# Kernel tuning notes

Hardware: AMD Instinct MI355X
Metric: run time of the kernel (lower is better)

## Reference

```python
import jax, jax.numpy as jnp
import numpy as np

# dims from VideoTokenizerConfig defaults + chosen video shape
B, T, IH, IW, C = 2, 16, 224, 224, 3
TP, PS, D, DFF, L, NH, K = 4, 16, 512, 2048, 6, 8, 8192
Tp, Hp, Wp = T // TP, IH // PS, IW // PS   # 4, 14, 14
S = Tp * Hp * Wp                           # 784 tokens
PIN = TP * PS * PS * C                     # 3072 patch elements
COMMIT = 0.25


def _ln(x, s, b):
    m = x.mean(-1, keepdims=True)
    v = ((x - m) ** 2).mean(-1, keepdims=True)
    return (x - m) / jnp.sqrt(v + 1e-6) * s + b


def _mha(x, Wqkv, bqkv, Wo, bo):
    b_, s_, d_ = x.shape
    hd = d_ // NH
    q = (x @ Wqkv[0] + bqkv[0]).reshape(b_, s_, NH, hd)
    k = (x @ Wqkv[1] + bqkv[1]).reshape(b_, s_, NH, hd)
    v = (x @ Wqkv[2] + bqkv[2]).reshape(b_, s_, NH, hd)
    att = jax.nn.softmax(jnp.einsum('bqhd,bkhd->bhqk', q, k) / jnp.sqrt(jnp.float32(hd)), axis=-1)
    o = jnp.einsum('bhqk,bkhd->bqhd', att, v).reshape(b_, s_, d_)
    return o @ Wo + bo


def _blocks(z, ln1s, ln1b, Wqkv, bqkv, Wo, bo, ln2s, ln2b, W1, b1, W2, b2):
    for i in range(L):  # small fixed layer count
        z = z + _mha(_ln(z, ln1s[i], ln1b[i]), Wqkv[i], bqkv[i], Wo[i], bo[i])
        h = jax.nn.gelu(_ln(z, ln2s[i], ln2b[i]) @ W1[i] + b1[i])
        z = z + h @ W2[i] + b2[i]
    return z


def _forward(video, e_patch_W, e_patch_b, e_pos_t, e_pos_h, e_pos_w,
             e_ln1_s, e_ln1_b, e_Wqkv, e_bqkv, e_Wo, e_bo, e_ln2_s, e_ln2_b,
             e_W1, e_b1, e_W2, e_b2, e_lnf_s, e_lnf_b, e_cb_W, e_cb_b,
             codebook,
             d_cb_W, d_cb_b, d_pos_t, d_pos_h, d_pos_w,
             d_ln1_s, d_ln1_b, d_Wqkv, d_bqkv, d_Wo, d_bo, d_ln2_s, d_ln2_b,
             d_W1, d_b1, d_W2, d_b2, d_lnf_s, d_lnf_b, d_px_W, d_px_b):
    # ---- encoder: 3D patchify ----
    v = video.reshape(B, Tp, TP, Hp, PS, Wp, PS, C)
    v = v.transpose(0, 1, 3, 5, 2, 4, 6, 7).reshape(B, Tp, Hp, Wp, PIN)
    z = v @ e_patch_W + e_patch_b
    z = z + e_pos_t + e_pos_h + e_pos_w
    z = z.reshape(B, S, D)
    z = _blocks(z, e_ln1_s, e_ln1_b, e_Wqkv, e_bqkv, e_Wo, e_bo,
                e_ln2_s, e_ln2_b, e_W1, e_b1, e_W2, e_b2)
    z = _ln(z, e_lnf_s, e_lnf_b)
    z_e = z @ e_cb_W + e_cb_b                      # [B,S,D]
    # ---- VQ quantize ----
    flat = z_e.reshape(-1, D)                      # [B*S, D]
    d2 = (flat ** 2).sum(1, keepdims=True) + (codebook ** 2).sum(1) - 2.0 * flat @ codebook.T
    idx = jnp.argmin(d2, axis=1)                   # [B*S]
    z_q = codebook[idx].reshape(z_e.shape)
    commit = jnp.mean((jax.lax.stop_gradient(z_q) - z_e) ** 2)
    cb_loss = jnp.mean((z_q - jax.lax.stop_gradient(z_e)) ** 2)
    z_q = z_e + jax.lax.stop_gradient(z_q - z_e)   # straight-through
    counts = jnp.zeros((K,), flat.dtype).at[idx].add(1.0)
    p = counts / idx.shape[0]                      # == mean(one_hot, axis=0)
    perplexity = jnp.exp(-jnp.sum(p * jnp.log(p + 1e-10)))
    # ---- decoder ----
    zd = z_q.reshape(B, Tp, Hp, Wp, D) @ d_cb_W + d_cb_b
    zd = zd + d_pos_t + d_pos_h + d_pos_w
    zd = zd.reshape(B, S, D)
    zd = _blocks(zd, d_ln1_s, d_ln1_b, d_Wqkv, d_bqkv, d_Wo, d_bo,
                 d_ln2_s, d_ln2_b, d_W1, d_b1, d_W2, d_b2)
    zd = _ln(zd, d_lnf_s, d_lnf_b)
    px = zd.reshape(B, Tp, Hp, Wp, D) @ d_px_W + d_px_b
    px = px.reshape(B, Tp, Hp, Wp, TP, PS, PS, C)
    recon = px.transpose(0, 1, 4, 2, 5, 3, 6, 7).reshape(B, T, IH, IW, C)
    return recon, idx.reshape(B, Tp, Hp, Wp), commit, cb_loss, perplexity


def setup_inputs() -> dict:
    key = jax.random.key(0)
    ks = iter(jax.random.split(key, 48))
    def nrm(shape, s=0.02):
        return (s * jax.random.normal(next(ks), shape)).astype(jnp.float32)
    z = lambda shape: jnp.zeros(shape, jnp.float32)
    o = lambda shape: jnp.ones(shape, jnp.float32)
    inp = {}
    inp['video'] = jax.random.normal(next(ks), (B, T, IH, IW, C), jnp.float32)
    # encoder params
    inp['e_patch_W'] = nrm((PIN, D)); inp['e_patch_b'] = z((D,))
    inp['e_pos_t'] = nrm((1, Tp, 1, 1, D)); inp['e_pos_h'] = nrm((1, 1, Hp, 1, D)); inp['e_pos_w'] = nrm((1, 1, 1, Wp, D))
    inp['e_ln1_s'] = o((L, D)); inp['e_ln1_b'] = z((L, D))
    inp['e_Wqkv'] = nrm((L, 3, D, D)); inp['e_bqkv'] = z((L, 3, D))
    inp['e_Wo'] = nrm((L, D, D)); inp['e_bo'] = z((L, D))
    inp['e_ln2_s'] = o((L, D)); inp['e_ln2_b'] = z((L, D))
    inp['e_W1'] = nrm((L, D, DFF)); inp['e_b1'] = z((L, DFF))
    inp['e_W2'] = nrm((L, DFF, D)); inp['e_b2'] = z((L, D))
    inp['e_lnf_s'] = o((D,)); inp['e_lnf_b'] = z((D,))
    inp['e_cb_W'] = nrm((D, D)); inp['e_cb_b'] = z((D,))
    inp['codebook'] = nrm((K, D))
    # decoder params
    inp['d_cb_W'] = nrm((D, D)); inp['d_cb_b'] = z((D,))
    inp['d_pos_t'] = nrm((1, Tp, 1, 1, D)); inp['d_pos_h'] = nrm((1, 1, Hp, 1, D)); inp['d_pos_w'] = nrm((1, 1, 1, Wp, D))
    inp['d_ln1_s'] = o((L, D)); inp['d_ln1_b'] = z((L, D))
    inp['d_Wqkv'] = nrm((L, 3, D, D)); inp['d_bqkv'] = z((L, 3, D))
    inp['d_Wo'] = nrm((L, D, D)); inp['d_bo'] = z((L, D))
    inp['d_ln2_s'] = o((L, D)); inp['d_ln2_b'] = z((L, D))
    inp['d_W1'] = nrm((L, D, DFF)); inp['d_b1'] = z((L, DFF))
    inp['d_W2'] = nrm((L, DFF, D)); inp['d_b2'] = z((L, D))
    inp['d_lnf_s'] = o((D,)); inp['d_lnf_b'] = z((D,))
    inp['d_px_W'] = nrm((D, PIN)); inp['d_px_b'] = z((PIN,))
    return inp


def reference(video, e_patch_W, e_patch_b, e_pos_t, e_pos_h, e_pos_w,
              e_ln1_s, e_ln1_b, e_Wqkv, e_bqkv, e_Wo, e_bo, e_ln2_s, e_ln2_b,
              e_W1, e_b1, e_W2, e_b2, e_lnf_s, e_lnf_b, e_cb_W, e_cb_b,
              codebook,
              d_cb_W, d_cb_b, d_pos_t, d_pos_h, d_pos_w,
              d_ln1_s, d_ln1_b, d_Wqkv, d_bqkv, d_Wo, d_bo, d_ln2_s, d_ln2_b,
              d_W1, d_b1, d_W2, d_b2, d_lnf_s, d_lnf_b, d_px_W, d_px_b):
    return _forward(video, e_patch_W, e_patch_b, e_pos_t, e_pos_h, e_pos_w,
                    e_ln1_s, e_ln1_b, e_Wqkv, e_bqkv, e_Wo, e_bo, e_ln2_s, e_ln2_b,
                    e_W1, e_b1, e_W2, e_b2, e_lnf_s, e_lnf_b, e_cb_W, e_cb_b,
                    codebook,
                    d_cb_W, d_cb_b, d_pos_t, d_pos_h, d_pos_w,
                    d_ln1_s, d_ln1_b, d_Wqkv, d_bqkv, d_Wo, d_bo, d_ln2_s, d_ln2_b,
                    d_W1, d_b1, d_W2, d_b2, d_lnf_s, d_lnf_b, d_px_W, d_px_b)
```

## Files before the change

### kernel.cpp

```cpp
#include <hip/hip_runtime.h>
#include <math.h>

#define Bq    2
#define Dq    512
#define DFFq  2048
#define Lq    6
#define NHq   8
#define HDq   64
#define Kq    8192
#define Sq    784
#define PINq  3072
#define TOKq  1568
#define RECN  4816896L

#define OFF_BIG  0L
#define SZ_BIG   12845056L
#define OFF_Z    (OFF_BIG + SZ_BIG)
#define OFF_XLN  (OFF_Z    + 802816L)
#define OFF_QKV  (OFF_XLN  + 802816L)
#define OFF_ATTO (OFF_QKV  + 2408448L)
#define OFF_H    (OFF_ATTO + 802816L)
#define OFF_ZE   (OFF_H    + 3211264L)
#define OFF_ZQ   (OFF_ZE   + 802816L)
#define OFF_CN   (OFF_ZQ   + 802816L)
#define OFF_IDX  (OFF_CN   + 8192L)
#define OFF_CNT  (OFF_IDX  + 1568L)
#define OFF_PART (OFF_CNT  + 8192L)
#define OFF_MIN  (OFF_PART + 1568L)
#define OFF_END  (OFF_MIN  + 3136L)

#define CEXT 802816L

typedef short bf16x8 __attribute__((ext_vector_type(8)));
typedef float f32x4  __attribute__((ext_vector_type(4)));
typedef unsigned short u16;
typedef unsigned long long u64;

#define XLO 802816L
#define QLO 2408448L
#define ALO 802816L
#define HLO 3211264L
#define PLO 4816896L
#define ZLO 802816L
#define CBLO 4194304L

__device__ __forceinline__ float wave_sum(float v) {
    #pragma unroll
    for (int o = 32; o; o >>= 1) v += __shfl_xor(v, o);
    return v;
}
__device__ __forceinline__ float gelu_f(float x) {
    float u = 0.7978845608028654f * (x + 0.044715f * x * x * x);
    float a = fabsf(u);
    float t = __expf(-2.0f * a);
    float th = (1.0f - t) / (1.0f + t);
    th = copysignf(th, u);
    return 0.5f * x * (1.0f + th);
}
__device__ __forceinline__ void split_f32(float x, u16& h, u16& l) {
    unsigned u = __float_as_uint(x);
    unsigned t = u + 0x7fffu + ((u >> 16) & 1u);
    h = (u16)(t >> 16);
    float r = x - __uint_as_float((t >> 16) << 16);
    l = (u16)(__float_as_uint(r) >> 16);
}
__device__ __forceinline__ void gload16(const u16* g, u16* l) {
    __builtin_amdgcn_global_load_lds(
        (const __attribute__((address_space(1))) void*)g,
        (__attribute__((address_space(3))) void*)l,
        16, 0, 0);
}

__global__ __launch_bounds__(256)
void wconv_t(const float* __restrict__ W, int ldw, int Kd,
             u16* __restrict__ WT, long loT, long soW, long soT)
{
    __shared__ u16 Lh[32][33], Ll[32][33];
    const float* Wp = W + (long)blockIdx.z * soW;
    u16* Tp = WT + (long)blockIdx.z * soT;
    int k0 = blockIdx.x << 5, n0 = blockIdx.y << 5;
    int t = threadIdx.x;
    int r = t >> 3, c4 = (t & 7) << 2;
    float4 v = *(const float4*)(Wp + (long)(k0 + r) * ldw + n0 + c4);
    u16 h, l;
    split_f32(v.x, h, l); Lh[c4+0][r] = h; Ll[c4+0][r] = l;
    split_f32(v.y, h, l); Lh[c4+1][r] = h; Ll[c4+1][r] = l;
    split_f32(v.z, h, l); Lh[c4+2][r] = h; Ll[c4+2][r] = l;
    split_f32(v.w, h, l); Lh[c4+3][r] = h; Ll[c4+3][r] = l;
    __syncthreads();
    int n = t >> 3, kc = (t & 7) << 2;
    u16* dst = Tp + (long)(n0 + n) * Kd + k0 + kc;
    u16 oh[4] = {Lh[n][kc], Lh[n][kc+1], Lh[n][kc+2], Lh[n][kc+3]};
    u16 ol[4] = {Ll[n][kc], Ll[n][kc+1], Ll[n][kc+2], Ll[n][kc+3]};
    *(uint2*)dst = *(uint2*)oh;
    *(uint2*)(dst + loT) = *(uint2*)ol;
}

__global__ __launch_bounds__(256)
void wconv4(const float* __restrict__ Wqkv, const float* __restrict__ Wo,
            const float* __restrict__ W1, const float* __restrict__ W2,
            u16* __restrict__ dst)
{
    __shared__ u16 Lh[32][33], Ll[32][33];
    int id = blockIdx.x;
    const float* W; int ldw, Kd, kblk, nblk; u16* Tp; long loT;
    if (id < 768) {
        int z = id >> 8, rid = id & 255;
        kblk = rid & 15; nblk = rid >> 4;
        W = Wqkv + (long)z * 262144; ldw = 512; Kd = 512;
        Tp = dst + (long)z * 262144; loT = 786432;
    } else if (id < 1024) {
        int rid = id - 768; kblk = rid & 15; nblk = rid >> 4;
        W = Wo; ldw = 512; Kd = 512; Tp = dst + 1572864; loT = 262144;
    } else if (id < 2048) {
        int rid = id - 1024; kblk = rid & 15; nblk = rid >> 4;
        W = W1; ldw = 2048; Kd = 512; Tp = dst + 2097152; loT = 1048576;
    } else {
        int rid = id - 2048; kblk = rid & 63; nblk = rid >> 6;
        W = W2; ldw = 512; Kd = 2048; Tp = dst + 4194304; loT = 1048576;
    }
    int k0 = kblk << 5, n0 = nblk << 5;
    int t = threadIdx.x;
    int r = t >> 3, c4 = (t & 7) << 2;
    float4 v = *(const float4*)(W + (long)(k0 + r) * ldw + n0 + c4);
    u16 h, l;
    split_f32(v.x, h, l); Lh[c4+0][r] = h; Ll[c4+0][r] = l;
    split_f32(v.y, h, l); Lh[c4+1][r] = h; Ll[c4+1][r] = l;
    split_f32(v.z, h, l); Lh[c4+2][r] = h; Ll[c4+2][r] = l;
    split_f32(v.w, h, l); Lh[c4+3][r] = h; Ll[c4+3][r] = l;
    __syncthreads();
    int n = t >> 3, kc = (t & 7) << 2;
    u16* d = Tp + (long)(n0 + n) * Kd + k0 + kc;
    u16 oh[4] = {Lh[n][kc], Lh[n][kc+1], Lh[n][kc+2], Lh[n][kc+3]};
    u16 ol[4] = {Ll[n][kc], Ll[n][kc+1], Ll[n][kc+2], Ll[n][kc+3]};
    *(uint2*)d = *(uint2*)oh;
    *(uint2*)(d + loT) = *(uint2*)ol;
}

__global__ __launch_bounds__(256)
void splitp(const float* __restrict__ X, u16* __restrict__ Y, long lo, long n4)
{
    long i = (long)blockIdx.x * 256 + threadIdx.x;
    if (i >= n4) return;
    float4 v = *(const float4*)(X + i * 4);
    u16 h[4], l[4];
    split_f32(v.x, h[0], l[0]); split_f32(v.y, h[1], l[1]);
    split_f32(v.z, h[2], l[2]); split_f32(v.w, h[3], l[3]);
    *(uint2*)(Y + i * 4) = *(uint2*)h;
    *(uint2*)(Y + lo + i * 4) = *(uint2*)l;
}

template<int MATH, int LV>
__global__ __launch_bounds__(256)
void gemm_bb(const u16* __restrict__ A, long rsA, long loA, long soA, long siA,
             const u16* __restrict__ B, long rsB, long loB, long soB, long siB,
             const float* __restrict__ bias, long siBias,
             const float* __restrict__ extra,
             float* __restrict__ Cf, int ldc, long soC, long siC,
             u16* __restrict__ Cb, int rsC, long loC,
             float* __restrict__ part, long pstride,
             int M, int N, int K, float alpha,
             int bdiv, int ksplit, int klen, int gx)
{
    constexpr int OFF_BH = (LV >= 2) ? 8192 : 4096;
    __shared__ u16 SH[LV == 3 ? 16384 : (LV == 2 ? 12288 : 8192)];
    const int zb2 = blockIdx.z;
    const int zk = zb2 % ksplit, zb = zb2 / ksplit;
    const int zo = zb / bdiv, zi = zb - zo * bdiv;
    A += zo * soA + zi * siA;
    B += zo * soB + zi * siB;
    const float* bi = bias ? bias + zi * siBias : nullptr;

    const int nwg = gridDim.x;
    int orig = blockIdx.x;
    int qq = nwg >> 3, rr = nwg & 7;
    int xcd = orig & 7, sidx = orig >> 3;
    int wgid = (xcd < rr ? xcd * (qq + 1) : rr * (qq + 1) + (xcd - rr) * qq) + sidx;
    const int m0 = (wgid % gx) << 6, n0 = (wgid / gx) << 6;

    const int t = threadIdx.x;
    const int kbeg = zk * klen;
    int kend = kbeg + klen; if (kend > K) kend = K;

    const int w = t >> 6, lane = t & 63;
    const int wm = w >> 1, wn = w & 1;
    const int l15 = lane & 15, g = lane >> 4;
    const int wq = w << 9;

    const int csrc = ((t & 3) + ((t >> 3) & 7)) & 3;
    int arow = m0 + (t >> 2); if (arow > M - 1) arow = M - 1;
    const u16* Apr = A + (long)arow * rsA + (csrc << 3);
    const u16* Bpr = B + (long)(n0 + (t >> 2)) * rsB + (csrc << 3);

    f32x4 acc[2][2] = {};

    for (int k0 = kbeg; k0 < kend; k0 += 64) {
        gload16(Apr + k0,            &SH[wq]);
        if (LV >= 2) gload16(Apr + k0 + loA,      &SH[4096 + wq]);
        gload16(Bpr + k0,            &SH[OFF_BH + wq]);
        if (LV == 3) gload16(Bpr + k0 + loB, &SH[12288 + wq]);
        gload16(Apr + k0 + 32,       &SH[2048 + wq]);
        if (LV >= 2) gload16(Apr + k0 + 32 + loA, &SH[4096 + 2048 + wq]);
        gload16(Bpr + k0 + 32,       &SH[OFF_BH + 2048 + wq]);
        if (LV == 3) gload16(Bpr + k0 + 32 + loB, &SH[12288 + 2048 + wq]);
        __syncthreads();

        #pragma unroll
        for (int sub = 0; sub < 2; ++sub) {
            const int so = sub << 11;
            bf16x8 ah[2], al2[2], bh2[2], bl2[2];
            #pragma unroll
            for (int mi = 0; mi < 2; ++mi) {
                int row = (wm << 5) + (mi << 4) + l15;
                int off = (row << 5) + (((g - (row >> 1)) & 3) << 3);
                ah[mi]  = *(const bf16x8*)&SH[so + off];
                if (LV >= 2) al2[mi] = *(const bf16x8*)&SH[4096 + so + off];
            }
            #pragma unroll
            for (int ni = 0; ni < 2; ++ni) {
                int row = (wn << 5) + (ni << 4) + l15;
                int off = (row << 5) + (((g - (row >> 1)) & 3) << 3);
                bh2[ni] = *(const bf16x8*)&SH[OFF_BH + so + off];
                if (LV == 3) bl2[ni] = *(const bf16x8*)&SH[12288 + so + off];
            }
            #pragma unroll
            for (int mi = 0; mi < 2; ++mi)
                #pragma unroll
                for (int ni = 0; ni < 2; ++ni) {
                    acc[mi][ni] = __builtin_amdgcn_mfma_f32_16x16x32_bf16(ah[mi], bh2[ni], acc[mi][ni], 0, 0, 0);
                    if (LV == 3) acc[mi][ni] = __builtin_amdgcn_mfma_f32_16x16x32_bf16(ah[mi], bl2[ni], acc[mi][ni], 0, 0, 0);
                    if (LV >= 2) acc[mi][ni] = __builtin_amdgcn_mfma_f32_16x16x32_bf16(al2[mi], bh2[ni], acc[mi][ni], 0, 0, 0);
                }
        }
        __syncthreads();
    }

    if (ksplit > 1) {
        float* P = part + (long)zk * pstride + zo * soC + zi * siC;
        #pragma unroll
        for (int mi = 0; mi < 2; ++mi)
            #pragma unroll
            for (int ni = 0; ni < 2; ++ni) {
                int gn = n0 + (wn << 5) + (ni << 4) + l15;
                if (gn >= N) continue;
                int gmb = m0 + (wm << 5) + (mi << 4) + (g << 2);
                #pragma unroll
                for (int r = 0; r < 4; ++r) {
                    int gm = gmb + r;
                    if (gm < M) P[(long)gm * ldc + gn] = acc[mi][ni][r];
                }
            }
        return;
    }
    if (MATH == 0) {
        float* Co = Cf + zo * soC + zi * siC;
        #pragma unroll
        for (int mi = 0; mi < 2; ++mi)
            #pragma unroll
            for (int ni = 0; ni < 2; ++ni) {
                int gn = n0 + (wn << 5) + (ni << 4) + l15;
                if (gn >= N) continue;
                int gmb = m0 + (wm << 5) + (mi << 4) + (g << 2);
                #pragma unroll
                for (int r = 0; r < 4; ++r) {
                    int gm = gmb + r;
                    if (gm >= M) continue;
                    Co[(long)gm * ldc + gn] = alpha * acc[mi][ni][r] + (bi ? bi[gn] : 0.0f);
                }
            }
    } else {
        u16* Cu = Cb + zo * soC + zi * siC;
        #pragma unroll
        for (int mi = 0; mi < 2; ++mi)
            #pragma unroll
            for (int ni = 0; ni < 2; ++ni) {
                int gn = n0 + (wn << 5) + (ni << 4) + l15;
                if (gn >= N) continue;
                int gmb = m0 + (wm << 5) + (mi << 4) + (g << 2);
                #pragma unroll
                for (int r = 0; r < 4; ++r) {
                    int gm = gmb + r;
                    if (gm >= M) continue;
                    float v = acc[mi][ni][r] + bi[gn];
                    if (MATH == 2) v = gelu_f(v);
                    u16 h, l; split_f32(v, h, l);
                    Cu[(long)gm * rsC + gn] = h;
                    Cu[(long)gm * rsC + gn + loC] = l;
                }
            }
    }
}

__global__ __launch_bounds__(256)
void gemm_d2w(const u16* __restrict__ A, long rsA, long loA,
              const u16* __restrict__ B, long rsB, long loB,
              const float* __restrict__ extra, u64* __restrict__ mb,
              int M, int N, int K, int gx)
{
    __shared__ u16 SH[24576];
    const int nwg = gridDim.x;
    int orig = blockIdx.x;
    int qq = nwg >> 3, rr = nwg & 7;
    int xcd = orig & 7, sidx = orig >> 3;
    int wgid = (xcd < rr ? xcd * (qq + 1) : rr * (qq + 1) + (xcd - rr) * qq) + sidx;
    const int m0 = (wgid % gx) << 6, n0 = (wgid / gx) << 7;

    const int t = threadIdx.x;
    const int w = t >> 6, lane = t & 63;
    const int wm = w >> 1, wn = w & 1;
    const int l15 = lane & 15, g = lane >> 4;
    const int wq = w << 9;

    const int csrc = ((t & 3) + ((t >> 3) & 7)) & 3;
    int arow = m0 + (t >> 2); if (arow > M - 1) arow = M - 1;
    const u16* Apr = A + (long)arow * rsA + (csrc << 3);
    const u16* Bpr0 = B + (long)(n0 + (t >> 2)) * rsB + (csrc << 3);
    const u16* Bpr1 = B + (long)(n0 + 64 + (t >> 2)) * rsB + (csrc << 3);

    f32x4 acc[2][4] = {};

    for (int k0 = 0; k0 < K; k0 += 64) {
        gload16(Apr + k0,             &SH[wq]);
        gload16(Apr + k0 + 32,        &SH[2048 + wq]);
        gload16(Apr + k0 + loA,       &SH[4096 + wq]);
        gload16(Apr + k0 + 32 + loA,  &SH[4096 + 2048 + wq]);
        gload16(Bpr0 + k0,            &SH[8192 + wq]);
        gload16(Bpr1 + k0,            &SH[8192 + 2048 + wq]);
        gload16(Bpr0 + k0 + 32,       &SH[12288 + wq]);
        gload16(Bpr1 + k0 + 32,       &SH[12288 + 2048 + wq]);
        gload16(Bpr0 + k0 + loB,      &SH[16384 + wq]);
        gload16(Bpr1 + k0 + loB,      &SH[16384 + 2048 + wq]);
        gload16(Bpr0 + k0 + 32 + loB, &SH[20480 + wq]);
        gload16(Bpr1 + k0 + 32 + loB, &SH[20480 + 2048 + wq]);
        __syncthreads();

        #pragma unroll
        for (int sub = 0; sub < 2; ++sub) {
            const int soA = sub << 11;
            const int soB = sub << 12;
            bf16x8 ah[2], al2[2], bh2[4], bl2[4];
            #pragma unroll
            for (int mi = 0; mi < 2; ++mi) {
                int row = (wm << 5) + (mi << 4) + l15;
                int off = (row << 5) + (((g - (row >> 1)) & 3) << 3);
                ah[mi]  = *(const bf16x8*)&SH[soA + off];
                al2[mi] = *(const bf16x8*)&SH[4096 + soA + off];
            }
            #pragma unroll
            for (int ni = 0; ni < 4; ++ni) {
                int row = (wn << 6) + (ni << 4) + l15;
                int off = (row << 5) + (((g - (row >> 1)) & 3) << 3);
                bh2[ni] = *(const bf16x8*)&SH[8192 + soB + off];
                bl2[ni] = *(const bf16x8*)&SH[16384 + soB + off];
            }
            #pragma unroll
            for (int mi = 0; mi < 2; ++mi)
                #pragma unroll
                for (int ni = 0; ni < 4; ++ni) {
                    acc[mi][ni] = __builtin_amdgcn_mfma_f32_16x16x32_bf16(ah[mi],  bh2[ni], acc[mi][ni], 0, 0, 0);
                    acc[mi][ni] = __builtin_amdgcn_mfma_f32_16x16x32_bf16(ah[mi],  bl2[ni], acc[mi][ni], 0, 0, 0);
                    acc[mi][ni] = __builtin_amdgcn_mfma_f32_16x16x32_bf16(al2[mi], bh2[ni], acc[mi][ni], 0, 0, 0);
                }
        }
        __syncthreads();
    }

    #pragma unroll
    for (int mi = 0; mi < 2; ++mi) {
        #pragma unroll
        for (int r = 0; r < 4; ++r) {
            u64 best = 0xFFFFFFFFFFFFFFFFULL;
            #pragma unroll
            for (int ni = 0; ni < 4; ++ni) {
                int gn = n0 + (wn << 6) + (ni << 4) + l15;
                float v = extra[gn] - 2.0f * acc[mi][ni][r];
                unsigned ub = __float_as_uint(v);
                ub = ub ^ ((ub >> 31) ? 0xFFFFFFFFu : 0x80000000u);
                u64 pk = ((u64)ub << 32) | (unsigned)gn;
                best = pk < best ? pk : best;
            }
            #pragma unroll
            for (int sft = 1; sft <= 8; sft <<= 1) {
                u64 o = __shfl_xor(best, sft);
                best = o < best ? o : best;
            }
            if (l15 == 0) {
                int gm = m0 + (wm << 5) + (mi << 4) + (g << 2) + r;
                if (gm < M) atomicMin(&mb[gm], best);
            }
        }
    }
}

#define KP 72
#define VP 40
#define CHR 196
template<bool X2>
__global__ __launch_bounds__(256)
void flash_kernel(const u16* __restrict__ qkv, float* __restrict__ O4, float* __restrict__ ML)
{
    __shared__ u16 Kh[32 * KP], Kl[32 * KP];
    __shared__ u16 Vh[64 * VP], Vl[64 * VP];
    __shared__ u16 Ph[64 * VP], Pl[64 * VP];

    const int qb = blockIdx.x, bh = blockIdx.y, ch = blockIdx.z;
    const int b = bh >> 3, h = bh & 7;
    const int jbeg = ch * CHR, jend = jbeg + CHR;
    const int t = threadIdx.x, w = t >> 6, lane = t & 63;
    const int l15 = lane & 15, g = lane >> 4;
    const long base = (long)b * 784 * 1536;
    const u16* Qg = qkv + base + h * 64;
    const u16* Kg = qkv + base + 512 + h * 64;
    const u16* Vg = qkv + base + 1024 + h * 64;

    const int q0 = qb << 6;
    int qr = q0 + w * 16 + l15; if (qr > 783) qr = 783;
    const u16* Qp = Qg + (long)qr * 1536 + g * 8;
    bf16x8 qh[2], ql[2];
    qh[0] = *(const bf16x8*)(Qp);
    qh[1] = *(const bf16x8*)(Qp + 32);
    ql[0] = *(const bf16x8*)(Qp + QLO);
    ql[1] = *(const bf16x8*)(Qp + QLO + 32);

    f32x4 O[4] = {};
    float m_[4] = {-1e30f, -1e30f, -1e30f, -1e30f};
    float l_[4] = {};

    const int srow = t >> 3, sc = (t & 7) << 3;

    for (int j0 = jbeg; j0 < jend; j0 += 32) {
        {
            int jr = j0 + srow;
            if (jr < jend) {
                const u16* Kp = Kg + (long)jr * 1536 + sc;
                *(uint4*)&Kh[srow * KP + sc] = *(const uint4*)(Kp);
                if (!X2) *(uint4*)&Kl[srow * KP + sc] = *(const uint4*)(Kp + QLO);
                const u16* Vp = Vg + (long)jr * 1536 + sc;
                u16 th[8], tl[8];
                *(uint4*)th = *(const uint4*)Vp;
                if (!X2) *(uint4*)tl = *(const uint4*)(Vp + QLO);
                #pragma unroll
                for (int e = 0; e < 8; ++e) {
                    Vh[(sc + e) * VP + srow] = th[e];
                    if (!X2) Vl[(sc + e) * VP + srow] = tl[e];
                }
            } else {
                uint4 zz = {0, 0, 0, 0};
                *(uint4*)&Kh[srow * KP + sc] = zz;
                if (!X2) *(uint4*)&Kl[srow * KP + sc] = zz;
                #pragma unroll
                for (int e = 0; e < 8; ++e) {
                    Vh[(sc + e) * VP + srow] = 0;
                    if (!X2) Vl[(sc + e) * VP + srow] = 0;
                }
            }
        }
        __syncthreads();

        f32x4 S[2] = {};
        #pragma unroll
        for (int f = 0; f < 2; ++f) {
            #pragma unroll
            for (int ks = 0; ks < 2; ++ks) {
                bf16x8 kh = *(const bf16x8*)&Kh[(f * 16 + l15) * KP + ks * 32 + g * 8];
                S[f] = __builtin_amdgcn_mfma_f32_16x16x32_bf16(qh[ks], kh, S[f], 0, 0, 0);
                if (!X2) {
                    bf16x8 kl = *(const bf16x8*)&Kl[(f * 16 + l15) * KP + ks * 32 + g * 8];
                    S[f] = __builtin_amdgcn_mfma_f32_16x16x32_bf16(qh[ks], kl, S[f], 0, 0, 0);
                }
                S[f] = __builtin_amdgcn_mfma_f32_16x16x32_bf16(ql[ks], kh, S[f], 0, 0, 0);
            }
        }

        float p[2][4];
        #pragma unroll
        for (int f = 0; f < 2; ++f) {
            bool ok = (j0 + f * 16 + l15) < jend;
            #pragma unroll
            for (int r = 0; r < 4; ++r)
                p[f][r] = ok ? S[f][r] * 0.125f : -1e30f;
        }
        #pragma unroll
        for (int r = 0; r < 4; ++r) {
            float pm = fmaxf(p[0][r], p[1][r]);
            pm = fmaxf(pm, __shfl_xor(pm, 1)); pm = fmaxf(pm, __shfl_xor(pm, 2));
            pm = fmaxf(pm, __shfl_xor(pm, 4)); pm = fmaxf(pm, __shfl_xor(pm, 8));
            float mn = fmaxf(m_[r], pm);
            float scl = __expf(m_[r] - mn);
            float rs = 0.f;
            #pragma unroll
            for (int f = 0; f < 2; ++f) { float e = __expf(p[f][r] - mn); p[f][r] = e; rs += e; }
            rs += __shfl_xor(rs, 1); rs += __shfl_xor(rs, 2);
            rs += __shfl_xor(rs, 4); rs += __shfl_xor(rs, 8);
            l_[r] = l_[r] * scl + rs;
            m_[r] = mn;
            O[0][r] *= scl; O[1][r] *= scl; O[2][r] *= scl; O[3][r] *= scl;
        }

        #pragma unroll
        for (int f = 0; f < 2; ++f)
            #pragma unroll
            for (int r = 0; r < 4; ++r) {
                u16 hh, ll; split_f32(p[f][r], hh, ll);
                int row = w * 16 + g * 4 + r;
                Ph[row * VP + f * 16 + l15] = hh;
                Pl[row * VP + f * 16 + l15] = ll;
            }

        bf16x8 pah = *(const bf16x8*)&Ph[(w * 16 + l15) * VP + g * 8];
        bf16x8 pal = *(const bf16x8*)&Pl[(w * 16 + l15) * VP + g * 8];
        #pragma unroll
        for (int f = 0; f < 4; ++f) {
            bf16x8 vh = *(const bf16x8*)&Vh[(f * 16 + l15) * VP + g * 8];
            O[f] = __builtin_amdgcn_mfma_f32_16x16x32_bf16(pah, vh, O[f], 0, 0, 0);
            O[f] = __builtin_amdgcn_mfma_f32_16x16x32_bf16(pal, vh, O[f], 0, 0, 0);
            if (!X2) {
                bf16x8 vl = *(const bf16x8*)&Vl[(f * 16 + l15) * VP + g * 8];
                O[f] = __builtin_amdgcn_mfma_f32_16x16x32_bf16(pah, vl, O[f], 0, 0, 0);
            }
        }
        __syncthreads();
    }

    #pragma unroll
    for (int r = 0; r < 4; ++r) {
        int q = q0 + w * 16 + g * 4 + r;
        if (q >= 784) continue;
        long rowi = ((long)ch * 16 + bh) * 784 + q;
        if (l15 == 0) { ML[rowi * 2] = m_[r]; ML[rowi * 2 + 1] = l_[r]; }
        #pragma unroll
        for (int f = 0; f < 4; ++f)
            O4[rowi * 64 + f * 16 + l15] = O[f][r];
    }
}

__global__ __launch_bounds__(256)
void flash_combine(const float* __restrict__ O4, const float* __restrict__ ML,
                   u16* __restrict__ atto)
{
    int wave = threadIdx.x >> 6, lane = threadIdx.x & 63;
    int row = (blockIdx.x << 2) + wave;
    int bh = row / 784, q = row - bh * 784;
    int b = bh >> 3, h = bh & 7;
    float mm[4], ll[4];
    float M = -1e30f;
    #pragma unroll
    for (int c = 0; c < 4; ++c) {
        long ri = ((long)c * 16 + bh) * 784 + q;
        mm[c] = ML[ri * 2]; ll[c] = ML[ri * 2 + 1];
        M = fmaxf(M, mm[c]);
    }
    float L = 0.f, sc[4];
    #pragma unroll
    for (int c = 0; c < 4; ++c) { sc[c] = __expf(mm[c] - M); L += sc[c] * ll[c]; }
    float o = 0.f;
    #pragma unroll
    for (int c = 0; c < 4; ++c)
        o += O4[(((long)c * 16 + bh) * 784 + q) * 64 + lane] * sc[c];
    o /= L;
    u16 hh, lo2; split_f32(o, hh, lo2);
    long off = ((long)b * 784 + q) * 512 + h * 64 + lane;
    atto[off] = hh; atto[off + ALO] = lo2;
}

template<int MATH>
__global__ __launch_bounds__(256)
void reduce_k(const float* __restrict__ part, long pstride, int ks,
              const float* __restrict__ bias, int ldc,
              float* __restrict__ Cf, u16* __restrict__ Cb, long loC, long total)
{
    long i = (long)blockIdx.x * 256 + threadIdx.x;
    if (i >= total) return;
    float s = 0.f;
    for (int k = 0; k < ks; ++k) s += part[(long)k * pstride + i];
    int col = (int)(i % ldc);
    float v = s + (bias ? bias[col] : 0.0f);
    if (MATH == 3) { Cf[i] = v; u16 h, l; split_f32(v, h, l); Cb[i] = h; Cb[i + loC] = l; }
    else { float g = gelu_f(v); u16 h, l; split_f32(g, h, l); Cb[i] = h; Cb[i + loC] = l; }
}

__global__ __launch_bounds__(256)
void redln(const float* __restrict__ part, long pstride, int ks,
           const float* __restrict__ bias,
           float* __restrict__ z,
           const float* __restrict__ s, const float* __restrict__ b,
           u16* __restrict__ y, long lo)
{
    int wave = threadIdx.x >> 6, lane = threadIdx.x & 63;
    int row = (blockIdx.x << 2) + wave;
    int c0 = lane << 3;
    long base = (long)row * 512 + c0;
    float a[8] = {};
    for (int k = 0; k < ks; ++k) {
        const float* p = part + (long)k * pstride + base;
        float4 p0 = *(const float4*)p, p1 = *(const float4*)(p + 4);
        a[0]+=p0.x; a[1]+=p0.y; a[2]+=p0.z; a[3]+=p0.w;
        a[4]+=p1.x; a[5]+=p1.y; a[6]+=p1.z; a[7]+=p1.w;
    }
    float4 b0 = *(const float4*)(bias + c0), b1 = *(const float4*)(bias + c0 + 4);
    a[0]+=b0.x; a[1]+=b0.y; a[2]+=b0.z; a[3]+=b0.w;
    a[4]+=b1.x; a[5]+=b1.y; a[6]+=b1.z; a[7]+=b1.w;
    float4 z0 = *(const float4*)(z + base), z1 = *(const float4*)(z + base + 4);
    float v[8] = { z0.x+a[0], z0.y+a[1], z0.z+a[2], z0.w+a[3],
                   z1.x+a[4], z1.y+a[5], z1.z+a[6], z1.w+a[7] };
    float4 o0, o1;
    o0.x=v[0]; o0.y=v[1]; o0.z=v[2]; o0.w=v[3];
    o1.x=v[4]; o1.y=v[5]; o1.z=v[6]; o1.w=v[7];
    *(float4*)(z + base) = o0; *(float4*)(z + base + 4) = o1;
    float sum = v[0]+v[1]+v[2]+v[3]+v[4]+v[5]+v[6]+v[7];
    sum = wave_sum(sum);
    float m = sum * (1.0f / 512.0f);
    float var = 0.f;
    float d[8];
    #pragma unroll
    for (int j = 0; j < 8; ++j) { d[j] = v[j] - m; var += d[j]*d[j]; }
    var = wave_sum(var);
    float rstd = 1.0f / sqrtf(var * (1.0f / 512.0f) + 1e-6f);
    u16 hh[8], ll[8];
    #pragma unroll
    for (int j = 0; j < 8; ++j)
        split_f32(d[j] * rstd * s[c0+j] + b[c0+j], hh[j], ll[j]);
    *(uint4*)(y + base) = *(uint4*)hh;
    *(uint4*)(y + lo + base) = *(uint4*)ll;
}

__global__ __launch_bounds__(256)
void redposln(const float* __restrict__ part, long pstride, int ks,
              const float* __restrict__ bias,
              const float* __restrict__ pt, const float* __restrict__ ph,
              const float* __restrict__ pw,
              float* __restrict__ z,
              const float* __restrict__ s, const float* __restrict__ b,
              u16* __restrict__ y, long lo)
{
    int wave = threadIdx.x >> 6, lane = threadIdx.x & 63;
    int row = (blockIdx.x << 2) + wave;
    int c0 = lane << 3;
    long base = (long)row * 512 + c0;
    int r = row % 784;
    int wp = r % 14, hh2 = (r / 14) % 14, tp = r / 196;
    float v[8] = {};
    for (int k = 0; k < ks; ++k) {
        const float* p = part + (long)k * pstride + base;
        float4 p0 = *(const float4*)p, p1 = *(const float4*)(p + 4);
        v[0]+=p0.x; v[1]+=p0.y; v[2]+=p0.z; v[3]+=p0.w;
        v[4]+=p1.x; v[5]+=p1.y; v[6]+=p1.z; v[7]+=p1.w;
    }
    const float* ptp = pt + tp * 512 + c0;
    const float* php = ph + hh2 * 512 + c0;
    const float* pwp = pw + wp * 512 + c0;
    #pragma unroll
    for (int j = 0; j < 8; ++j) v[j] += bias[c0+j] + ptp[j] + php[j] + pwp[j];
    float4 o0, o1;
    o0.x=v[0]; o0.y=v[1]; o0.z=v[2]; o0.w=v[3];
    o1.x=v[4]; o1.y=v[5]; o1.z=v[6]; o1.w=v[7];
    *(float4*)(z + base) = o0; *(float4*)(z + base + 4) = o1;
    float sum = v[0]+v[1]+v[2]+v[3]+v[4]+v[5]+v[6]+v[7];
    sum = wave_sum(sum);
    float m = sum * (1.0f / 512.0f);
    float var = 0.f; float d[8];
    #pragma unroll
    for (int j = 0; j < 8; ++j) { d[j] = v[j] - m; var += d[j]*d[j]; }
    var = wave_sum(var);
    float rstd = 1.0f / sqrtf(var * (1.0f / 512.0f) + 1e-6f);
    u16 hh[8], ll[8];
    #pragma unroll
    for (int j = 0; j < 8; ++j)
        split_f32(d[j] * rstd * s[c0+j] + b[c0+j], hh[j], ll[j]);
    *(uint4*)(y + base) = *(uint4*)hh;
    *(uint4*)(y + lo + base) = *(uint4*)ll;
}

__global__ __launch_bounds__(256)
void cnorm_kernel(const float* __restrict__ cb, float* __restrict__ cn)
{
    int wave = threadIdx.x >> 6, lane = threadIdx.x & 63;
    int row = (blockIdx.x << 2) + wave;
    if (row >= Kq) return;
    const float* cr = cb + (long)row * Dq;
    float4 v0 = *(const float4*)(cr + (lane << 2));
    float4 v1 = *(const float4*)(cr + 256 + (lane << 2));
    float ss = v0.x*v0.x+v0.y*v0.y+v0.z*v0.z+v0.w*v0.w
             + v1.x*v1.x+v1.y*v1.y+v1.z*v1.z+v1.w*v1.w;
    ss = wave_sum(ss);
    if (lane == 0) cn[row] = ss;
}

__global__ void patchify_kernel(const float* __restrict__ video, u16* __restrict__ patches)
{
    long i = (long)blockIdx.x * 256 + threadIdx.x;
    if (i >= (long)TOKq * PINq) return;
    int row = (int)(i / PINq), col = (int)(i - (long)row * PINq);
    int c = col % 3; int q = col / 3;
    int pw = q & 15; q >>= 4;
    int ph = q & 15; int tpin = q >> 4;
    int wp = row % 14; int r2 = row / 14;
    int hp = r2 % 14; r2 /= 14;
    int tp = r2 & 3; int b = r2 >> 2;
    int tt = tp * 4 + tpin;
    int ih = hp * 16 + ph, iw = wp * 16 + pw;
    float v = video[(((long)(b * 16 + tt) * 224 + ih) * 224 + iw) * 3 + c];
    u16 h, l; split_f32(v, h, l);
    patches[i] = h; patches[PLO + i] = l;
}

__global__ void unpatchify_kernel(const float* __restrict__ px, float* __restrict__ out)
{
    long o = (long)blockIdx.x * 256 + threadIdx.x;
    if (o >= RECN) return;
    int c = (int)(o % 3); long r = o / 3;
    int iw = (int)(r % 224); r /= 224;
    int ih = (int)(r % 224); r /= 224;
    int tt = (int)(r % 16); int b = (int)(r / 16);
    int tp = tt >> 2, tpin = tt & 3;
    int hp = ih >> 4, ph = ih & 15;
    int wp = iw >> 4, pw = iw & 15;
    long prow = ((long)(b * 4 + tp) * 14 + hp) * 14 + wp;
    int pcol = ((tpin * 16 + ph) * 16 + pw) * 3 + c;
    out[o] = px[prow * PINq + pcol];
}

__global__ __launch_bounds__(256)
void zq_kernel(const float* __restrict__ cb, const u64* __restrict__ minb,
               const float* __restrict__ ze, u16* __restrict__ zqp, long lo,
               float* __restrict__ part, float* __restrict__ counts,
               float* __restrict__ out_idx)
{
    int tok = blockIdx.x;
    int id = (int)(minb[tok] & 0xFFFFFFFFULL);
    const float* c = cb + (long)id * Dq;
    const float* z = ze + (long)tok * Dq;
    float ss = 0.f;
    for (int d = threadIdx.x; d < Dq; d += 256) {
        float cv = c[d];
        u16 h, l; split_f32(cv, h, l);
        zqp[(long)tok * Dq + d] = h;
        zqp[lo + (long)tok * Dq + d] = l;
        float df = cv - z[d];
        ss += df * df;
    }
    float wsum = wave_sum(ss);
    __shared__ float sw[4];
    if ((threadIdx.x & 63) == 0) sw[threadIdx.x >> 6] = wsum;
    __syncthreads();
    if (threadIdx.x == 0) {
        part[tok] = sw[0] + sw[1] + sw[2] + sw[3];
        atomicAdd(&counts[id], 1.0f);
        out_idx[tok] = (float)id;
    }
}

__global__ __launch_bounds__(256)
void scalars_kernel(const float* __restrict__ part, const float* __restrict__ counts,
                    float* __restrict__ out)
{
    float se = 0.f;
    for (int t = threadIdx.x; t < TOKq; t += 256) se += part[t];
    float pl = 0.f;
    for (int k = threadIdx.x; k < Kq; k += 256) {
        float p = counts[k] * (1.0f / 1568.0f);
        pl += p * logf(p + 1e-10f);
    }
    float wse = wave_sum(se), wpl = wave_sum(pl);
    __shared__ float s1[4], s2[4];
    if ((threadIdx.x & 63) == 0) { s1[threadIdx.x >> 6] = wse; s2[threadIdx.x >> 6] = wpl; }
    __syncthreads();
    if (threadIdx.x == 0) {
        float sse = s1[0] + s1[1] + s1[2] + s1[3];
        float plo = s2[0] + s2[1] + s2[2] + s2[3];
        float commit = sse / 802816.0f;
        out[RECN + 1568 + 0] = commit;
        out[RECN + 1568 + 1] = commit;
        out[RECN + 1568 + 2] = expf(-plo);
    }
}

template<int LVA, int LVF, bool FX2>
static void block_fwd(hipStream_t st, float* z, float* big, float* hbuf,
                      u16* xlnu, u16* qkvu, u16* attou, u16* hbu, u16* wscr,
                      const float* Wqkv, const float* bqkv,
                      const float* Wo, const float* bo,
                      const float* ln2s, const float* ln2b,
                      const float* W1, const float* b1,
                      const float* W2, const float* b2,
                      const float* nls, const float* nlb)
{
    wconv4<<<3072, 256, 0, st>>>(Wqkv, Wo, W1, W2, wscr);
    gemm_bb<4, LVA><<<dim3(600, 1, 1), 256, 0, st>>>(
        xlnu, Dq, XLO, 0, 0,
        wscr, Dq, 786432, 0, 0,
        bqkv, 0, nullptr,
        nullptr, 0, 0, 0,
        qkvu, 1536, QLO,
        nullptr, 0,
        TOKq, 1536, Dq, 1.0f, 1, 1, Dq, 25);
    flash_kernel<FX2><<<dim3(13, 16, 4), 256, 0, st>>>(qkvu, big, big + 3211264L);
    flash_combine<<<3136, 256, 0, st>>>(big, big + 3211264L, attou);
    gemm_bb<0, LVA><<<dim3(200, 1, 4), 256, 0, st>>>(
        attou, Dq, ALO, 0, 0,
        wscr + 1572864, Dq, 262144, 0, 0,
        nullptr, 0, nullptr,
        nullptr, Dq, 0, 0,
        nullptr, 0, 0,
        hbuf, CEXT,
        TOKq, Dq, Dq, 1.0f, 1, 4, 128, 25);
    redln<<<392, 256, 0, st>>>(hbuf, CEXT, 4, bo, z, ln2s, ln2b, xlnu, XLO);
    gemm_bb<2, LVF><<<dim3(800, 1, 1), 256, 0, st>>>(
        xlnu, Dq, XLO, 0, 0,
        wscr + 2097152, Dq, 1048576, 0, 0,
        b1, 0, nullptr,
        nullptr, 0, 0, 0,
        hbu, DFFq, HLO,
        nullptr, 0,
        TOKq, DFFq, Dq, 1.0f, 1, 1, Dq, 25);
    gemm_bb<0, LVF><<<dim3(200, 1, 4), 256, 0, st>>>(
        hbu, DFFq, HLO, 0, 0,
        wscr + 4194304, DFFq, 1048576, 0, 0,
        nullptr, 0, nullptr,
        nullptr, Dq, 0, 0,
        nullptr, 0, 0,
        big, CEXT,
        TOKq, Dq, DFFq, 1.0f, 1, 4, 512, 25);
    redln<<<392, 256, 0, st>>>(big, CEXT, 4, b2, z, nls, nlb, xlnu, XLO);
}

extern "C" void kernel_launch(void* const* d_in, const int* in_sizes, int n_in,
                              void* d_out, int out_size, void* d_ws, size_t ws_size,
                              hipStream_t stream)
{
    (void)in_sizes; (void)n_in; (void)out_size;
    if (ws_size < (size_t)OFF_END * sizeof(float)) return;

    const float* video = (const float*)d_in[0];
    const float* epW   = (const float*)d_in[1];  const float* epb   = (const float*)d_in[2];
    const float* ept   = (const float*)d_in[3];  const float* ephp  = (const float*)d_in[4];
    const float* epwp  = (const float*)d_in[5];
    const float* eln1s = (const float*)d_in[6];  const float* eln1b = (const float*)d_in[7];
    const float* eWqkv = (const float*)d_in[8];  const float* ebqkv = (const float*)d_in[9];
    const float* eWo   = (const float*)d_in[10]; const float* ebo   = (const float*)d_in[11];
    const float* eln2s = (const float*)d_in[12]; const float* eln2b = (const float*)d_in[13];
    const float* eW1   = (const float*)d_in[14]; const float* eb1   = (const float*)d_in[15];
    const float* eW2   = (const float*)d_in[16]; const float* eb2   = (const float*)d_in[17];
    const float* elnfs = (const float*)d_in[18]; const float* elnfb = (const float*)d_in[19];
    const float* ecbW  = (const float*)d_in[20]; const float* ecbb  = (const float*)d_in[21];
    const float* cbook = (const float*)d_in[22];
    const float* dcbW  = (const float*)d_in[23]; const float* dcbb  = (const float*)d_in[24];
    const float* dpt   = (const float*)d_in[25]; const float* dphp  = (const float*)d_in[26];
    const float* dpwp  = (const float*)d_in[27];
    const float* dln1s = (const float*)d_in[28]; const float* dln1b = (const float*)d_in[29];
    const float* dWqkv = (const float*)d_in[30]; const float* dbqkv = (const float*)d_in[31];
    const float* dWo   = (const float*)d_in[32]; const float* dbo   = (const float*)d_in[33];
    const float* dln2s = (const float*)d_in[34]; const float* dln2b = (const float*)d_in[35];
    const float* dW1   = (const float*)d_in[36]; const float* db1   = (const float*)d_in[37];
    const float* dW2   = (const float*)d_in[38]; const float* db2   = (const float*)d_in[39];
    const float* dlnfs = (const float*)d_in[40]; const float* dlnfb = (const float*)d_in[41];
    const float* dpxW  = (const float*)d_in[42]; const float* dpxb  = (const float*)d_in[43];

    float* ws   = (float*)d_ws;
    float* big  = ws + OFF_BIG;
    float* z    = ws + OFF_Z;
    float* xln  = ws + OFF_XLN;
    float* qkv  = ws + OFF_QKV;
    float* atto = ws + OFF_ATTO;
    float* hbuf = ws + OFF_H;
    float* ze   = ws + OFF_ZE;
    float* zq   = ws + OFF_ZQ;
    float* cn   = ws + OFF_CN;
    float* cnt  = ws + OFF_CNT;
    float* part = ws + OFF_PART;
    u64*   minb = (u64*)(ws + OFF_MIN);
    float* out  = (float*)d_out;

    u16* xlnu  = (u16*)xln;
    u16* qkvu  = (u16*)qkv;
    u16* attou = (u16*)atto;
    u16* hbu   = (u16*)hbuf;
    u16* patu  = (u16*)big;
    u16* zqu   = (u16*)zq;
    u16* cbs   = (u16*)qkv;
    u16* wscr  = (u16*)(big + 9633792);

    hipMemsetAsync(cnt, 0, Kq * sizeof(float), stream);
    hipMemsetAsync(minb, 0xFF, TOKq * sizeof(u64), stream);
    cnorm_kernel<<<Kq / 4, 256, 0, stream>>>(cbook, cn);

    patchify_kernel<<<(int)(((long)TOKq * PINq + 255) / 256), 256, 0, stream>>>(video, patu);
    wconv_t<<<dim3(96, 16, 1), 256, 0, stream>>>(epW, Dq, PINq, wscr, 1572864, 0, 0);
    gemm_bb<0, 3><<<dim3(200, 1, 6), 256, 0, stream>>>(
        patu, PINq, PLO, 0, 0,
        wscr, PINq, 1572864, 0, 0,
        nullptr, 0, nullptr,
        nullptr, Dq, 0, 0,
        nullptr, 0, 0,
        big + PLO, CEXT,
        TOKq, Dq, PINq, 1.0f, 1, 6, 512, 25);
    redposln<<<392, 256, 0, stream>>>(big + PLO, CEXT, 6, epb, ept, ephp, epwp,
                                      z, eln1s, eln1b, xlnu, XLO);

    for (int l = 0; l < Lq; ++l) {
        const float* nls = (l < 5) ? eln1s + (l + 1) * Dq : elnfs;
        const float* nlb = (l < 5) ? eln1b + (l + 1) * Dq : elnfb;
        block_fwd<3, 3, false>(stream, z, big, hbuf, xlnu, qkvu, attou, hbu, wscr,
                         eWqkv + (long)l * 3 * Dq * Dq, ebqkv + l * 3 * Dq,
                         eWo + (long)l * Dq * Dq, ebo + l * Dq,
                         eln2s + l * Dq, eln2b + l * Dq,
                         eW1 + (long)l * Dq * DFFq, eb1 + l * DFFq,
                         eW2 + (long)l * DFFq * Dq, eb2 + l * Dq,
                         nls, nlb);
    }

    wconv_t<<<dim3(16, 16, 1), 256, 0, stream>>>(ecbW, Dq, Dq, wscr, 262144, 0, 0);
    gemm_bb<0, 3><<<dim3(200, 1, 2), 256, 0, stream>>>(
        xlnu, Dq, XLO, 0, 0,
        wscr, Dq, 262144, 0, 0,
        nullptr, 0, nullptr,
        nullptr, Dq, 0, 0,
        nullptr, 0, 0,
        big, CEXT,
        TOKq, Dq, Dq, 1.0f, 1, 2, 256, 25);
    reduce_k<3><<<(CEXT + 255) / 256, 256, 0, stream>>>(big, CEXT, 2, ecbb, Dq, ze, zqu, ZLO, CEXT);

    splitp<<<(int)(((long)Kq * Dq / 4 + 255) / 256), 256, 0, stream>>>(cbook, cbs, CBLO, (long)Kq * Dq / 4);
    gemm_d2w<<<dim3(1600, 1, 1), 256, 0, stream>>>(
        zqu, Dq, ZLO,
        cbs, Dq, CBLO,
        cn, minb,
        TOKq, Kq, Dq, 25);
    zq_kernel<<<TOKq, 256, 0, stream>>>(cbook, minb, ze, zqu, ZLO, part, cnt, out + RECN);
    scalars_kernel<<<1, 256, 0, stream>>>(part, cnt, out);

    wconv_t<<<dim3(16, 16, 1), 256, 0, stream>>>(dcbW, Dq, Dq, wscr, 262144, 0, 0);
    gemm_bb<0, 2><<<dim3(200, 1, 2), 256, 0, stream>>>(
        zqu, Dq, ZLO, 0, 0,
        wscr, Dq, 262144, 0, 0,
        nullptr, 0, nullptr,
        nullptr, Dq, 0, 0,
        nullptr, 0, 0,
        big, CEXT,
        TOKq, Dq, Dq, 1.0f, 1, 2, 256, 25);
    redposln<<<392, 256, 0, stream>>>(big, CEXT, 2, dcbb, dpt, dphp, dpwp,
                                      z, dln1s, dln1b, xlnu, XLO);

    for (int l = 0; l < Lq; ++l) {
        const float* nls = (l < 5) ? dln1s + (l + 1) * Dq : dlnfs;
        const float* nlb = (l < 5) ? dln1b + (l + 1) * Dq : dlnfb;
        block_fwd<2, 1, true>(stream, z, big, hbuf, xlnu, qkvu, attou, hbu, wscr,
                        dWqkv + (long)l * 3 * Dq * Dq, dbqkv + l * 3 * Dq,
                        dWo + (long)l * Dq * Dq, dbo + l * Dq,
                        dln2s + l * Dq, dln2b + l * Dq,
                        dW1 + (long)l * Dq * DFFq, db1 + l * DFFq,
                        dW2 + (long)l * DFFq * Dq, db2 + l * Dq,
                        nls, nlb);
    }

    wconv_t<<<dim3(16, 96, 1), 256, 0, stream>>>(dpxW, PINq, Dq, wscr, 1572864, 0, 0);
    gemm_bb<0, 2><<<dim3(1200, 1, 1), 256, 0, stream>>>(
        xlnu, Dq, XLO, 0, 0,
        wscr, Dq, 1572864, 0, 0,
        dpxb, 0, nullptr,
        big, PINq, 0, 0,
        nullptr, 0, 0,
        nullptr, 0,
        TOKq, PINq, Dq, 1.0f, 1, 1, Dq, 25);
    unpatchify_kernel<<<(int)((RECN + 255) / 256), 256, 0, stream>>>(big, out);
}
```

Measured before the change: 1.695 ms.

## Fuse codebook prep, codebook-proj epilogue, and unpatchify into GEMM epilogues

Merges the codebook norm and split kernels into one pass over the codebook. The encoder-to-codebook projection now runs without split-K and writes fp32 and split outputs directly in a new epilogue, dropping the reduce kernel. The final pixel projection scatters results straight into the video output layout, removing the unpatchify kernel and its intermediate buffer. The trade-off is fewer blocks on the small projection and strided scattered writes in the final GEMM epilogue.

Measured after the change: 1.738 ms. +2.5%, slower.

```diff
diff --git a/kernel.cpp b/kernel.cpp
--- a/kernel.cpp
+++ b/kernel.cpp
@@ -138,16 +138,25 @@
 }
 
 __global__ __launch_bounds__(256)
-void splitp(const float* __restrict__ X, u16* __restrict__ Y, long lo, long n4)
-{
-    long i = (long)blockIdx.x * 256 + threadIdx.x;
-    if (i >= n4) return;
-    float4 v = *(const float4*)(X + i * 4);
-    u16 h[4], l[4];
-    split_f32(v.x, h[0], l[0]); split_f32(v.y, h[1], l[1]);
-    split_f32(v.z, h[2], l[2]); split_f32(v.w, h[3], l[3]);
-    *(uint2*)(Y + i * 4) = *(uint2*)h;
-    *(uint2*)(Y + lo + i * 4) = *(uint2*)l;
+void cbprep(const float* __restrict__ cb, float* __restrict__ cn, u16* __restrict__ cbs)
+{
+    int wave = threadIdx.x >> 6, lane = threadIdx.x & 63;
+    int row = (blockIdx.x << 2) + wave;
+    const float* cr = cb + (long)row * Dq;
+    int c0 = lane << 3;
+    float4 v0 = *(const float4*)(cr + c0);
+    float4 v1 = *(const float4*)(cr + c0 + 4);
+    float ss = v0.x*v0.x+v0.y*v0.y+v0.z*v0.z+v0.w*v0.w
+             + v1.x*v1.x+v1.y*v1.y+v1.z*v1.z+v1.w*v1.w;
+    ss = wave_sum(ss);
+    if (lane == 0) cn[row] = ss;
+    u16 h[8], l[8];
+    split_f32(v0.x, h[0], l[0]); split_f32(v0.y, h[1], l[1]);
+    split_f32(v0.z, h[2], l[2]); split_f32(v0.w, h[3], l[3]);
+    split_f32(v1.x, h[4], l[4]); split_f32(v1.y, h[5], l[5]);
+    split_f32(v1.z, h[6], l[6]); split_f32(v1.w, h[7], l[7]);
+    *(uint4*)(cbs + (long)row * Dq + c0) = *(uint4*)h;
+    *(uint4*)(cbs + CBLO + (long)row * Dq + c0) = *(uint4*)l;
 }
 
 template<int MATH, int LV>
@@ -266,6 +275,47 @@
                     int gm = gmb + r;
                     if (gm >= M) continue;
                     Co[(long)gm * ldc + gn] = alpha * acc[mi][ni][r] + (bi ? bi[gn] : 0.0f);
+                }
+            }
+    } else if (MATH == 3) {
+        #pragma unroll
+        for (int mi = 0; mi < 2; ++mi)
+            #pragma unroll
+            for (int ni = 0; ni < 2; ++ni) {
+                int gn = n0 + (wn << 5) + (ni << 4) + l15;
+                if (gn >= N) continue;
+                int gmb = m0 + (wm << 5) + (mi << 4) + (g << 2);
+                #pragma unroll
+                for (int r = 0; r < 4; ++r) {
+                    int gm = gmb + r;
+                    if (gm >= M) continue;
+                    float v = acc[mi][ni][r] + bi[gn];
+                    Cf[(long)gm * ldc + gn] = v;
+                    u16 h, l; split_f32(v, h, l);
+                    Cb[(long)gm * rsC + gn] = h;
+                    Cb[(long)gm * rsC + gn + loC] = l;
+                }
+            }
+    } else if (MATH == 6) {
+        #pragma unroll
+        for (int mi = 0; mi < 2; ++mi)
+            #pragma unroll
+            for (int ni = 0; ni < 2; ++ni) {
+                int gn = n0 + (wn << 5) + (ni << 4) + l15;
+                if (gn >= N) continue;
+                int c = gn % 3; int q = gn / 3;
+                int pw = q & 15, ph = (q >> 4) & 15, tpin = q >> 8;
+                int gmb = m0 + (wm << 5) + (mi << 4) + (g << 2);
+                #pragma unroll
+                for (int r = 0; r < 4; ++r) {
+                    int gm = gmb + r;
+                    if (gm >= M) continue;
+                    float v = acc[mi][ni][r] + bi[gn];
+                    int wp = gm % 14; int t1 = gm / 14;
+                    int hp = t1 % 14; int t2 = t1 / 14;
+                    int tp = t2 & 3, b = t2 >> 2;
+                    long o = ((((long)(b * 16 + tp * 4 + tpin) * 224) + hp * 16 + ph) * 224 + wp * 16 + pw) * 3 + c;
+                    Cf[o] = v;
                 }
             }
     } else {
@@ -563,22 +613,6 @@
     atto[off] = hh; atto[off + ALO] = lo2;
 }
 
-template<int MATH>
-__global__ __launch_bounds__(256)
-void reduce_k(const float* __restrict__ part, long pstride, int ks,
-              const float* __restrict__ bias, int ldc,
-              float* __restrict__ Cf, u16* __restrict__ Cb, long loC, long total)
-{
-    long i = (long)blockIdx.x * 256 + threadIdx.x;
-    if (i >= total) return;
-    float s = 0.f;
-    for (int k = 0; k < ks; ++k) s += part[(long)k * pstride + i];
-    int col = (int)(i % ldc);
-    float v = s + (bias ? bias[col] : 0.0f);
-    if (MATH == 3) { Cf[i] = v; u16 h, l; split_f32(v, h, l); Cb[i] = h; Cb[i + loC] = l; }
-    else { float g = gelu_f(v); u16 h, l; split_f32(g, h, l); Cb[i] = h; Cb[i + loC] = l; }
-}
-
 __global__ __launch_bounds__(256)
 void redln(const float* __restrict__ part, long pstride, int ks,
            const float* __restrict__ bias,
@@ -671,21 +705,6 @@
     *(uint4*)(y + lo + base) = *(uint4*)ll;
 }
 
-__global__ __launch_bounds__(256)
-void cnorm_kernel(const float* __restrict__ cb, float* __restrict__ cn)
-{
-    int wave = threadIdx.x >> 6, lane = threadIdx.x & 63;
-    int row = (blockIdx.x << 2) + wave;
-    if (row >= Kq) return;
-    const float* cr = cb + (long)row * Dq;
-    float4 v0 = *(const float4*)(cr + (lane << 2));
-    float4 v1 = *(const float4*)(cr + 256 + (lane << 2));
-    float ss = v0.x*v0.x+v0.y*v0.y+v0.z*v0.z+v0.w*v0.w
-             + v1.x*v1.x+v1.y*v1.y+v1.z*v1.z+v1.w*v1.w;
-    ss = wave_sum(ss);
-    if (lane == 0) cn[row] = ss;
-}
-
 __global__ void patchify_kernel(const float* __restrict__ video, u16* __restrict__ patches)
 {
     long i = (long)blockIdx.x * 256 + threadIdx.x;
@@ -702,22 +721,6 @@
     float v = video[(((long)(b * 16 + tt) * 224 + ih) * 224 + iw) * 3 + c];
     u16 h, l; split_f32(v, h, l);
     patches[i] = h; patches[PLO + i] = l;
-}
-
-__global__ void unpatchify_kernel(const float* __restrict__ px, float* __restrict__ out)
-{
-    long o = (long)blockIdx.x * 256 + threadIdx.x;
-    if (o >= RECN) return;
-    int c = (int)(o % 3); long r = o / 3;
-    int iw = (int)(r % 224); r /= 224;
-    int ih = (int)(r % 224); r /= 224;
-    int tt = (int)(r % 16); int b = (int)(r / 16);
-    int tp = tt >> 2, tpin = tt & 3;
-    int hp = ih >> 4, ph = ih & 15;
-    int wp = iw >> 4, pw = iw & 15;
-    long prow = ((long)(b * 4 + tp) * 14 + hp) * 14 + wp;
-    int pcol = ((tpin * 16 + ph) * 16 + pw) * 3 + c;
-    out[o] = px[prow * PINq + pcol];
 }
 
 __global__ __launch_bounds__(256)
@@ -882,7 +885,6 @@
 
     hipMemsetAsync(cnt, 0, Kq * sizeof(float), stream);
     hipMemsetAsync(minb, 0xFF, TOKq * sizeof(u64), stream);
-    cnorm_kernel<<<Kq / 4, 256, 0, stream>>>(cbook, cn);
 
     patchify_kernel<<<(int)(((long)TOKq * PINq + 255) / 256), 256, 0, stream>>>(video, patu);
     wconv_t<<<dim3(96, 16, 1), 256, 0, stream>>>(epW, Dq, PINq, wscr, 1572864, 0, 0);
@@ -910,17 +912,16 @@
     }
 
     wconv_t<<<dim3(16, 16, 1), 256, 0, stream>>>(ecbW, Dq, Dq, wscr, 262144, 0, 0);
-    gemm_bb<0, 3><<<dim3(200, 1, 2), 256, 0, stream>>>(
+    gemm_bb<3, 3><<<dim3(200, 1, 1), 256, 0, stream>>>(
         xlnu, Dq, XLO, 0, 0,
         wscr, Dq, 262144, 0, 0,
-        nullptr, 0, nullptr,
-        nullptr, Dq, 0, 0,
-        nullptr, 0, 0,
-        big, CEXT,
-        TOKq, Dq, Dq, 1.0f, 1, 2, 256, 25);
-    reduce_k<3><<<(CEXT + 255) / 256, 256, 0, stream>>>(big, CEXT, 2, ecbb, Dq, ze, zqu, ZLO, CEXT);
-
-    splitp<<<(int)(((long)Kq * Dq / 4 + 255) / 256), 256, 0, stream>>>(cbook, cbs, CBLO, (long)Kq * Dq / 4);
+        ecbb, 0, nullptr,
+        ze, Dq, 0, 0,
+        zqu, Dq, ZLO,
+        nullptr, 0,
+        TOKq, Dq, Dq, 1.0f, 1, 1, Dq, 25);
+
+    cbprep<<<Kq / 4, 256, 0, stream>>>(cbook, cn, cbs);
     gemm_d2w<<<dim3(1600, 1, 1), 256, 0, stream>>>(
         zqu, Dq, ZLO,
         cbs, Dq, CBLO,
@@ -954,13 +955,12 @@
     }
 
     wconv_t<<<dim3(16, 96, 1), 256, 0, stream>>>(dpxW, PINq, Dq, wscr, 1572864, 0, 0);
-    gemm_bb<0, 2><<<dim3(1200, 1, 1), 256, 0, stream>>>(
+    gemm_bb<6, 2><<<dim3(1200, 1, 1), 256, 0, stream>>>(
         xlnu, Dq, XLO, 0, 0,
         wscr, Dq, 1572864, 0, 0,
         dpxb, 0, nullptr,
-        big, PINq, 0, 0,
+        out, PINq, 0, 0,
         nullptr, 0, 0,
         nullptr, 0,
         TOKq, PINq, Dq, 1.0f, 1, 1, Dq, 25);
-    unpatchify_kernel<<<(int)((RECN + 255) / 256), 256, 0, stream>>>(big, out);
-}
+}
```
